# Performance work log

Measured on AMD Instinct MI355X. Metric: run time of the kernel, lower is better.

## Reference

```python
import jax, jax.numpy as jnp
import numpy as np

B, S, E, H = 4, 2048, 1024, 16
HD = E // H  # 64


def setup_inputs() -> dict:
    key = jax.random.key(0)
    k1, k2, k3, k4, k5 = jax.random.split(key, 5)
    scale = 0.02
    return {
        "hidden_states": jax.random.normal(k1, (B, S, E), dtype=jnp.float32),
        "c_attn_w": jax.random.normal(k2, (E, 3 * E), dtype=jnp.float32) * scale,
        "c_attn_b": jnp.zeros((3 * E,), dtype=jnp.float32),
        "c_proj_w": jax.random.normal(k3, (E, E), dtype=jnp.float32) * scale,
        "c_proj_b": jnp.zeros((E,), dtype=jnp.float32),
    }


def reference(hidden_states, c_attn_w, c_attn_b, c_proj_w, c_proj_b):
    b, s, e = hidden_states.shape
    h, hd = H, HD
    # Conv1D: x @ W + b
    qkv = hidden_states @ c_attn_w + c_attn_b                     # [B,S,3E]
    # Faithful to source: split heads BEFORE splitting q/k/v
    qkv = qkv.reshape(b, s, h, 3 * hd).transpose(0, 2, 1, 3)      # [B,H,S,3*hd]
    q, k, v = jnp.split(qkv, 3, axis=-1)                          # each [B,H,S,hd]
    scores = jnp.einsum("bhqd,bhkd->bhqk", q, k) / (hd ** 0.5)    # [B,H,S,S]
    causal = jnp.tril(jnp.ones((s, s), dtype=bool))
    masked_bias = jnp.asarray(-10000.0, dtype=scores.dtype)
    scores = jnp.where(causal, scores, masked_bias)
    attn_weights = jax.nn.softmax(scores, axis=-1)                # [B,H,S,S]
    attn_out = jnp.einsum("bhqk,bhkd->bhqd", attn_weights, v)     # [B,H,S,hd]
    attn_out = attn_out.transpose(0, 2, 1, 3).reshape(b, s, e)    # merge heads
    out = attn_out @ c_proj_w + c_proj_b                          # [B,S,E]
    return out
```

## Files before the change

kernel.cpp:

```cpp
#include <hip/hip_runtime.h>

typedef __attribute__((ext_vector_type(8))) __bf16 bf16x8;
typedef __attribute__((ext_vector_type(2))) __bf16 bf16x2;
typedef __attribute__((ext_vector_type(8))) unsigned short u16x8;
typedef __attribute__((ext_vector_type(4))) float f32x4;
typedef __attribute__((ext_vector_type(16))) float f32x16;
typedef __attribute__((ext_vector_type(4))) unsigned int u32x4;
typedef unsigned short u16;
typedef unsigned int u32;

constexpr int Bb = 4, Ss = 2048, Ee = 1024, Hh = 16, HDd = 64;
constexpr int Mm = Bb * Ss;
constexpr int N3 = 3 * Ee;
constexpr float QSC = 0.18033688011112042f;
constexpr int BHSTRIDE = Ss * HDd;
constexpr float M0 = 8.0f;

__device__ __forceinline__ u16 f2bf(float f) {
  u32 u = __builtin_bit_cast(u32, f);
  u = (u + 0x7FFFu + ((u >> 16) & 1u)) >> 16;
  return (u16)u;
}
__device__ __forceinline__ u32 pk2(float a, float b) {
  bf16x2 t;
  t[0] = (__bf16)a;
  t[1] = (__bf16)b;
  return __builtin_bit_cast(u32, t);
}
__device__ __forceinline__ float ex2(float x) { return __builtin_exp2f(x); }

__device__ __forceinline__ void gload_lds16(const void* g, void* l) {
  __builtin_amdgcn_global_load_lds(
      (__attribute__((address_space(1))) void*)g,
      (__attribute__((address_space(3))) void*)l, 16, 0, 0);
}

__device__ __forceinline__ f32x4 mfma16(bf16x8 a, bf16x8 b, f32x4 c) {
  return __builtin_amdgcn_mfma_f32_16x16x32_bf16(a, b, c, 0, 0, 0);
}
__device__ __forceinline__ f32x16 mfma32(bf16x8 a, bf16x8 b, f32x16 c) {
  return __builtin_amdgcn_mfma_f32_32x32x16_bf16(a, b, c, 0, 0, 0);
}

__global__ void cast_x_kernel(const float* __restrict__ x, u16* __restrict__ xb, int n4) {
  int i = blockIdx.x * blockDim.x + threadIdx.x;
  int stride = gridDim.x * blockDim.x;
  for (; i < n4; i += stride) {
    float4 v = reinterpret_cast<const float4*>(x)[i];
    ushort4 o;
    o.x = f2bf(v.x); o.y = f2bf(v.y); o.z = f2bf(v.z); o.w = f2bf(v.w);
    reinterpret_cast<ushort4*>(xb)[i] = o;
  }
}

__global__ void transpose_cast_kernel(const float* __restrict__ W, u16* __restrict__ Wt,
                                      int K, int N) {
  __shared__ float tile[32][33];
  int n0 = blockIdx.x * 32, k0 = blockIdx.y * 32;
  int tx = threadIdx.x & 31, ty = threadIdx.x >> 5;
#pragma unroll
  for (int i = 0; i < 4; ++i)
    tile[ty + i * 8][tx] = W[(size_t)(k0 + ty + i * 8) * N + n0 + tx];
  __syncthreads();
#pragma unroll
  for (int i = 0; i < 4; ++i)
    Wt[(size_t)(n0 + ty + i * 8) * K + k0 + tx] = f2bf(tile[tx][ty + i * 8]);
}

template <int MODE>
__global__ __launch_bounds__(512, 1) void gemm8_kernel(
    const u16* __restrict__ A, const u16* __restrict__ Bt,
    const float* __restrict__ bias, int xtiles, int cpx,
    float* __restrict__ Cout, u16* __restrict__ Qr,
    u16* __restrict__ Kp, u16* __restrict__ Vp) {
  extern __shared__ __attribute__((aligned(16))) u16 dyn[];
  constexpr int K = 1024, NT = 16;

  int f = blockIdx.x;
  int swz = (f & 7) * cpx + (f >> 3);
  int bx = swz % xtiles, by = swz / xtiles;
  int m0 = by * 128, n0 = bx * 256;

  int tid = threadIdx.x, lane = tid & 63, wid = tid >> 6;
  int wr = wid >> 2, wc = wid & 3;
  int l7 = lane & 7, l8 = lane >> 3;
  int swcol = (l7 ^ l8) * 8;

  const u16* Ab = A + (size_t)(m0 + l8) * K + swcol;
  const u16* Bb = Bt + (size_t)(n0 + l8) * K + swcol;

  f32x4 acc[4][4];
  const f32x4 fz = {0.f, 0.f, 0.f, 0.f};
#pragma unroll
  for (int mi = 0; mi < 4; ++mi)
#pragma unroll
    for (int nj = 0; nj < 4; ++nj) acc[mi][nj] = fz;

  auto stageA = [&](int tt, int c) {
    int ch = wid * 2 + c;
    gload_lds16(Ab + (size_t)(8 * ch) * K + tt * 64,
                dyn + (tt & 1) * 8192 + ch * 512);
  };
  auto stageB = [&](int tt, int c) {
    int ch = wid * 4 + c;
    gload_lds16(Bb + (size_t)(8 * ch) * K + tt * 64,
                dyn + 16384 + (tt & 1) * 16384 + ch * 512);
  };

  stageA(0, 0); stageA(0, 1);
  stageB(0, 0); stageB(0, 1); stageB(0, 2); stageB(0, 3);

  for (int t = 0; t < NT; ++t) {
    const u16* Ar = dyn + (t & 1) * 8192;
    const u16* Br = dyn + 16384 + (t & 1) * 16384;
    bool pre = (t + 1 < NT);
    if (pre) {
      stageA(t + 1, 0); stageA(t + 1, 1); stageB(t + 1, 0);
      asm volatile("s_waitcnt vmcnt(3)" ::: "memory");
    } else {
      asm volatile("s_waitcnt vmcnt(0)" ::: "memory");
    }
    __builtin_amdgcn_sched_barrier(0);
    __builtin_amdgcn_s_barrier();
    __builtin_amdgcn_sched_barrier(0);
#pragma unroll
    for (int kk = 0; kk < 2; ++kk) {
      if (kk == 1 && pre) { stageB(t + 1, 1); stageB(t + 1, 2); stageB(t + 1, 3); }
      bf16x8 af[4], bfr[4];
      int kc = kk * 4 + (lane >> 4);
      int jsw = (kc ^ l7) << 3;
#pragma unroll
      for (int i = 0; i < 4; ++i) {
        int rowA = wr * 64 + i * 16 + (lane & 15);
        af[i] = *(const bf16x8*)&Ar[rowA * 64 + jsw];
        int rowB = wc * 64 + i * 16 + (lane & 15);
        bfr[i] = *(const bf16x8*)&Br[rowB * 64 + jsw];
      }
      __builtin_amdgcn_s_setprio(1);
#pragma unroll
      for (int mi = 0; mi < 4; ++mi)
#pragma unroll
        for (int nj = 0; nj < 4; ++nj)
          acc[mi][nj] = mfma16(af[mi], bfr[nj], acc[mi][nj]);
      __builtin_amdgcn_s_setprio(0);
      asm volatile("" ::: "memory");
      __builtin_amdgcn_s_barrier();
      asm volatile("" ::: "memory");
    }
  }

  if (MODE == 0) {
    int Nn = xtiles * 256;
#pragma unroll
    for (int nj = 0; nj < 4; ++nj) {
      int n = n0 + wc * 64 + nj * 16 + (lane & 15);
      float bn = bias[n];
#pragma unroll
      for (int mi = 0; mi < 4; ++mi)
#pragma unroll
        for (int r = 0; r < 4; ++r) {
          int m = m0 + wr * 64 + mi * 16 + (lane >> 4) * 4 + r;
          Cout[(size_t)m * Nn + n] = acc[mi][nj][r] + bn;
        }
    }
  } else {
    int gidx = bx * 4 + wc;
    int typ = gidx % 3, h = gidx / 3;
    int bb = m0 >> 11;
    size_t basebh = (size_t)(bb * 16 + h) * BHSTRIDE;
    float cs = (typ == 0) ? QSC : 1.0f;
#pragma unroll
    for (int nj = 0; nj < 4; ++nj) {
      int dl = nj * 16 + (lane & 15);
      float bn = bias[gidx * 64 + dl];
#pragma unroll
      for (int mi = 0; mi < 4; ++mi)
#pragma unroll
        for (int r = 0; r < 4; ++r) {
          int m = m0 + wr * 64 + mi * 16 + (lane >> 4) * 4 + r;
          int srw = m & 2047;
          u16 v = f2bf((acc[mi][nj][r] + bn) * cs);
          if (typ == 0) {
            Qr[basebh + (size_t)srw * 64 + dl] = v;
          } else if (typ == 1) {
            int tile = srw >> 6, rl = srw & 63;
            Kp[basebh + tile * 4096 + (rl >> 5) * 2048 + (dl >> 4) * 512 +
               ((dl >> 3) & 1) * 256 + (rl & 31) * 8 + (dl & 7)] = v;
          } else {
            int tile = srw >> 6;
            Vp[basebh + tile * 4096 + (dl >> 5) * 2048 + ((srw >> 4) & 3) * 512 +
               ((srw >> 3) & 1) * 256 + (dl & 31) * 8 + (srw & 7)] = v;
          }
        }
    }
  }
}

__global__ __launch_bounds__(256) void attn_kernel(const u16* __restrict__ Qr,
                                                   const u16* __restrict__ Kp,
                                                   const u16* __restrict__ Vp,
                                                   u16* __restrict__ aout) {
  __shared__ float mbuf[2][64][33];

  int bh = blockIdx.x;
  int j = gridDim.y - 1 - blockIdx.y;
  int tid = threadIdx.x, w = tid >> 6, lane = tid & 63;
  int hi = lane >> 5, ln31 = lane & 31;
  int qrow = 32 * j + ln31;
  int nt = (j >> 1) + 1;
  int par = (j & 1) ? 32 : 0;

  size_t basebh = (size_t)bh * BHSTRIDE;
  const u16* kp = Kp + basebh + (size_t)w * 4096 + hi * 256 + ln31 * 8;
  const u16* vp = Vp + basebh + (size_t)w * 4096 + hi * 256 + ln31 * 8;

  bf16x8 qf[4];
#pragma unroll
  for (int kc = 0; kc < 4; ++kc)
    qf[kc] = *(const bf16x8*)(Qr + basebh + (size_t)qrow * 64 + kc * 16 + hi * 8);

  f32x16 o[2];
#pragma unroll
  for (int dm = 0; dm < 2; ++dm)
#pragma unroll
    for (int e = 0; e < 16; ++e) o[dm][e] = 0.f;
  float lrun = 0.f;

  for (int t = w; t < nt; t += 4, kp += 4 * 4096, vp += 4 * 4096) {
    bf16x8 kf[2][4], vf[2][4];
#pragma unroll
    for (int mt = 0; mt < 2; ++mt)
#pragma unroll
      for (int kc = 0; kc < 4; ++kc)
        kf[mt][kc] = *(const bf16x8*)(kp + mt * 2048 + kc * 512);
#pragma unroll
    for (int dm = 0; dm < 2; ++dm)
#pragma unroll
      for (int kw = 0; kw < 4; ++kw)
        vf[dm][kw] = *(const bf16x8*)(vp + dm * 2048 + kw * 512);

    f32x16 sc[2];
#pragma unroll
    for (int mt = 0; mt < 2; ++mt)
#pragma unroll
      for (int e = 0; e < 16; ++e) sc[mt][e] = 0.f;
    __builtin_amdgcn_s_setprio(1);
#pragma unroll
    for (int mt = 0; mt < 2; ++mt)
#pragma unroll
      for (int kc = 0; kc < 4; ++kc)
        sc[mt] = mfma32(kf[mt][kc], qf[kc], sc[mt]);
    __builtin_amdgcn_s_setprio(0);

    if (t == nt - 1) {
#pragma unroll
      for (int mt = 0; mt < 2; ++mt)
#pragma unroll
        for (int r = 0; r < 16; ++r) {
          bool msk = (32 * mt + (r & 3) + 8 * (r >> 2) + 4 * hi) > (ln31 + par);
          sc[mt][r] = msk ? -__builtin_inff() : sc[mt][r];
        }
    }
    float s0a = 0.f, s1a = 0.f, s2a = 0.f, s3a = 0.f;
#pragma unroll
    for (int mt = 0; mt < 2; ++mt)
#pragma unroll
      for (int r = 0; r < 16; ++r) {
        float e = ex2(sc[mt][r] - M0);
        sc[mt][r] = e;
        if ((r & 3) == 0) s0a += e;
        else if ((r & 3) == 1) s1a += e;
        else if ((r & 3) == 2) s2a += e;
        else s3a += e;
      }
    float sum = (s0a + s1a) + (s2a + s3a);
    sum += __shfl_xor(sum, 32);
    lrun += sum;

#pragma unroll
    for (int kw = 0; kw < 4; ++kw) {
      int mt = kw >> 1, k8 = (kw & 1) * 8;
      u32 a0 = pk2(sc[mt][k8 + 0], sc[mt][k8 + 1]);
      u32 a1 = pk2(sc[mt][k8 + 2], sc[mt][k8 + 3]);
      u32 b0 = pk2(sc[mt][k8 + 4], sc[mt][k8 + 5]);
      u32 b1 = pk2(sc[mt][k8 + 6], sc[mt][k8 + 7]);
      u32 s0 = hi ? a0 : b0;
      u32 s1 = hi ? a1 : b1;
      u32 r0 = (u32)__shfl_xor((int)s0, 32);
      u32 r1 = (u32)__shfl_xor((int)s1, 32);
      u32x4 fw;
      fw.x = hi ? r0 : a0;
      fw.y = hi ? r1 : a1;
      fw.z = hi ? b0 : r0;
      fw.w = hi ? b1 : r1;
      bf16x8 pf = __builtin_bit_cast(bf16x8, fw);
      __builtin_amdgcn_s_setprio(1);
#pragma unroll
      for (int dm = 0; dm < 2; ++dm)
        o[dm] = mfma32(vf[dm][kw], pf, o[dm]);
      __builtin_amdgcn_s_setprio(0);
    }
  }

  if (w >= 2) {
    mbuf[w - 2][lane][0] = lrun;
#pragma unroll
    for (int dm = 0; dm < 2; ++dm)
#pragma unroll
      for (int e = 0; e < 16; ++e) mbuf[w - 2][lane][1 + dm * 16 + e] = o[dm][e];
  }
  __syncthreads();
  if (w < 2) {
    lrun += mbuf[w][lane][0];
#pragma unroll
    for (int dm = 0; dm < 2; ++dm)
#pragma unroll
      for (int e = 0; e < 16; ++e) o[dm][e] += mbuf[w][lane][1 + dm * 16 + e];
  }
  __syncthreads();
  if (w == 1) {
    mbuf[0][lane][0] = lrun;
#pragma unroll
    for (int dm = 0; dm < 2; ++dm)
#pragma unroll
      for (int e = 0; e < 16; ++e) mbuf[0][lane][1 + dm * 16 + e] = o[dm][e];
  }
  __syncthreads();
  if (w == 0) {
    lrun += mbuf[0][lane][0];
#pragma unroll
    for (int dm = 0; dm < 2; ++dm)
#pragma unroll
      for (int e = 0; e < 16; ++e) o[dm][e] += mbuf[0][lane][1 + dm * 16 + e];
    int b = bh >> 4, h = bh & 15;
    float inv = 1.f / lrun;
    u16* orow = aout + (size_t)(b * Ss + qrow) * Ee + h * HDd;
#pragma unroll
    for (int dm = 0; dm < 2; ++dm)
#pragma unroll
      for (int g = 0; g < 4; ++g) {
        ushort4 st;
        st.x = f2bf(o[dm][4 * g + 0] * inv);
        st.y = f2bf(o[dm][4 * g + 1] * inv);
        st.z = f2bf(o[dm][4 * g + 2] * inv);
        st.w = f2bf(o[dm][4 * g + 3] * inv);
        *(ushort4*)(orow + 32 * dm + 8 * g + 4 * hi) = st;
      }
  }
}

extern "C" void kernel_launch(void* const* d_in, const int* in_sizes, int n_in,
                              void* d_out, int out_size, void* d_ws, size_t ws_size,
                              hipStream_t stream) {
  const float* hs        = (const float*)d_in[0];
  const float* c_attn_w  = (const float*)d_in[1];
  const float* c_attn_b  = (const float*)d_in[2];
  const float* c_proj_w  = (const float*)d_in[3];
  const float* c_proj_b  = (const float*)d_in[4];
  float* out = (float*)d_out;

  char* ws = (char*)d_ws;
  size_t off = 0;
  u16* xb     = (u16*)(ws + off); off += (size_t)Mm * Ee * 2;
  u16* wqkvt  = (u16*)(ws + off); off += (size_t)N3 * Ee * 2;
  u16* wprojt = (u16*)(ws + off); off += (size_t)Ee * Ee * 2;
  u16* Qr     = (u16*)(ws + off); off += (size_t)64 * BHSTRIDE * 2;
  u16* Kp     = (u16*)(ws + off); off += (size_t)64 * BHSTRIDE * 2;
  u16* Vp     = (u16*)(ws + off); off += (size_t)64 * BHSTRIDE * 2;
  u16* aoutb  = (u16*)(ws + off); off += (size_t)Mm * Ee * 2;
  if (ws_size < off) return;

  (void)hipFuncSetAttribute(reinterpret_cast<const void*>(gemm8_kernel<1>),
                            hipFuncAttributeMaxDynamicSharedMemorySize, 98304);
  (void)hipFuncSetAttribute(reinterpret_cast<const void*>(gemm8_kernel<0>),
                            hipFuncAttributeMaxDynamicSharedMemorySize, 98304);

  cast_x_kernel<<<2048, 256, 0, stream>>>(hs, xb, Mm * Ee / 4);
  transpose_cast_kernel<<<dim3(N3 / 32, Ee / 32), 256, 0, stream>>>(c_attn_w, wqkvt, Ee, N3);
  transpose_cast_kernel<<<dim3(Ee / 32, Ee / 32), 256, 0, stream>>>(c_proj_w, wprojt, Ee, Ee);
  gemm8_kernel<1><<<768, 512, 98304, stream>>>(
      xb, wqkvt, c_attn_b, 12, 96, nullptr, Qr, Kp, Vp);
  attn_kernel<<<dim3(Bb * Hh, 64), 256, 0, stream>>>(Qr, Kp, Vp, aoutb);
  gemm8_kernel<0><<<256, 512, 98304, stream>>>(
      aoutb, wprojt, c_proj_b, 4, 32, out, nullptr, nullptr, nullptr);
}
```

Before: 171.7 us.

## Triple-buffer GEMM LDS pipeline and stage QKV epilogue through LDS for vector stores

```diff
diff --git a/kernel.cpp b/kernel.cpp
--- a/kernel.cpp
+++ b/kernel.cpp
@@ -68,13 +68,14 @@
 }
 
 template <int MODE>
-__global__ __launch_bounds__(512, 1) void gemm8_kernel(
+__global__ __launch_bounds__(512, 1) void gemm_pipe(
     const u16* __restrict__ A, const u16* __restrict__ Bt,
     const float* __restrict__ bias, int xtiles, int cpx,
     float* __restrict__ Cout, u16* __restrict__ Qr,
     u16* __restrict__ Kp, u16* __restrict__ Vp) {
   extern __shared__ __attribute__((aligned(16))) u16 dyn[];
   constexpr int K = 1024, NT = 16;
+  constexpr int BUFSTRIDE = 24576;
 
   int f = blockIdx.x;
   int swz = (f & 7) * cpx + (f >> 3);
@@ -96,58 +97,68 @@
 #pragma unroll
     for (int nj = 0; nj < 4; ++nj) acc[mi][nj] = fz;
 
-  auto stageA = [&](int tt, int c) {
+  auto STA = [&](int tt, int c) {
     int ch = wid * 2 + c;
-    gload_lds16(Ab + (size_t)(8 * ch) * K + tt * 64,
-                dyn + (tt & 1) * 8192 + ch * 512);
+    gload_lds16(Ab + (size_t)(ch * 8) * K + tt * 64,
+                dyn + (tt % 3) * BUFSTRIDE + ch * 512);
   };
-  auto stageB = [&](int tt, int c) {
+  auto STB = [&](int tt, int c) {
     int ch = wid * 4 + c;
-    gload_lds16(Bb + (size_t)(8 * ch) * K + tt * 64,
-                dyn + 16384 + (tt & 1) * 16384 + ch * 512);
+    gload_lds16(Bb + (size_t)(ch * 8) * K + tt * 64,
+                dyn + (tt % 3) * BUFSTRIDE + 8192 + ch * 512);
   };
-
-  stageA(0, 0); stageA(0, 1);
-  stageB(0, 0); stageB(0, 1); stageB(0, 2); stageB(0, 3);
+  auto LDA = [&](const u16* buf, int mi, int ks) -> bf16x8 {
+    int row = wr * 64 + mi * 16 + (lane & 15);
+    int j = ((ks * 4 + (lane >> 4)) ^ l7) * 8;
+    return *(const bf16x8*)&buf[row * 64 + j];
+  };
+  auto LDB = [&](const u16* buf, int ni, int ks) -> bf16x8 {
+    int row = wc * 64 + ni * 16 + (lane & 15);
+    int j = ((ks * 4 + (lane >> 4)) ^ l7) * 8;
+    return *(const bf16x8*)&buf[row * 64 + j];
+  };
+
+#pragma unroll
+  for (int c = 0; c < 2; ++c) STA(0, c);
+#pragma unroll
+  for (int c = 0; c < 4; ++c) STB(0, c);
+#pragma unroll
+  for (int c = 0; c < 2; ++c) STA(1, c);
+#pragma unroll
+  for (int c = 0; c < 4; ++c) STB(1, c);
 
   for (int t = 0; t < NT; ++t) {
-    const u16* Ar = dyn + (t & 1) * 8192;
-    const u16* Br = dyn + 16384 + (t & 1) * 16384;
-    bool pre = (t + 1 < NT);
-    if (pre) {
-      stageA(t + 1, 0); stageA(t + 1, 1); stageB(t + 1, 0);
-      asm volatile("s_waitcnt vmcnt(3)" ::: "memory");
-    } else {
+    const u16* Ar = dyn + (t % 3) * BUFSTRIDE;
+    const u16* Br = Ar + 8192;
+    if (t + 1 < NT)
+      asm volatile("s_waitcnt vmcnt(6)" ::: "memory");
+    else
       asm volatile("s_waitcnt vmcnt(0)" ::: "memory");
-    }
     __builtin_amdgcn_sched_barrier(0);
     __builtin_amdgcn_s_barrier();
     __builtin_amdgcn_sched_barrier(0);
+
+    bool pre2 = (t + 2) < NT;
 #pragma unroll
     for (int kk = 0; kk < 2; ++kk) {
-      if (kk == 1 && pre) { stageB(t + 1, 1); stageB(t + 1, 2); stageB(t + 1, 3); }
       bf16x8 af[4], bfr[4];
-      int kc = kk * 4 + (lane >> 4);
-      int jsw = (kc ^ l7) << 3;
-#pragma unroll
-      for (int i = 0; i < 4; ++i) {
-        int rowA = wr * 64 + i * 16 + (lane & 15);
-        af[i] = *(const bf16x8*)&Ar[rowA * 64 + jsw];
-        int rowB = wc * 64 + i * 16 + (lane & 15);
-        bfr[i] = *(const bf16x8*)&Br[rowB * 64 + jsw];
-      }
+#pragma unroll
+      for (int mi = 0; mi < 4; ++mi) af[mi] = LDA(Ar, mi, kk);
+#pragma unroll
+      for (int ni = 0; ni < 4; ++ni) bfr[ni] = LDB(Br, ni, kk);
+      if (kk == 0 && pre2) { STA(t + 2, 0); STA(t + 2, 1); }
+      if (kk == 1 && pre2) { STB(t + 2, 0); STB(t + 2, 1); STB(t + 2, 2); STB(t + 2, 3); }
       __builtin_amdgcn_s_setprio(1);
 #pragma unroll
       for (int mi = 0; mi < 4; ++mi)
 #pragma unroll
-        for (int nj = 0; nj < 4; ++nj)
-          acc[mi][nj] = mfma16(af[mi], bfr[nj], acc[mi][nj]);
+        for (int ni = 0; ni < 4; ++ni)
+          acc[mi][ni] = mfma16(af[mi], bfr[ni], acc[mi][ni]);
       __builtin_amdgcn_s_setprio(0);
       asm volatile("" ::: "memory");
-      __builtin_amdgcn_s_barrier();
-      asm volatile("" ::: "memory");
     }
   }
+  __syncthreads();
 
   if (MODE == 0) {
     int Nn = xtiles * 256;
@@ -164,34 +175,68 @@
         }
     }
   } else {
-    int gidx = bx * 4 + wc;
-    int typ = gidx % 3, h = gidx / 3;
+    int gi0 = bx * 4;
     int bb = m0 >> 11;
-    size_t basebh = (size_t)(bb * 16 + h) * BHSTRIDE;
-    float cs = (typ == 0) ? QSC : 1.0f;
-#pragma unroll
-    for (int nj = 0; nj < 4; ++nj) {
-      int dl = nj * 16 + (lane & 15);
-      float bn = bias[gidx * 64 + dl];
-#pragma unroll
-      for (int mi = 0; mi < 4; ++mi)
-#pragma unroll
-        for (int r = 0; r < 4; ++r) {
-          int m = m0 + wr * 64 + mi * 16 + (lane >> 4) * 4 + r;
-          int srw = m & 2047;
-          u16 v = f2bf((acc[mi][nj][r] + bn) * cs);
-          if (typ == 0) {
-            Qr[basebh + (size_t)srw * 64 + dl] = v;
-          } else if (typ == 1) {
-            int tile = srw >> 6, rl = srw & 63;
-            Kp[basebh + tile * 4096 + (rl >> 5) * 2048 + (dl >> 4) * 512 +
-               ((dl >> 3) & 1) * 256 + (rl & 31) * 8 + (dl & 7)] = v;
-          } else {
-            int tile = srw >> 6;
-            Vp[basebh + tile * 4096 + (dl >> 5) * 2048 + ((srw >> 4) & 3) * 512 +
-               ((srw >> 3) & 1) * 256 + (dl & 31) * 8 + (srw & 7)] = v;
+    int mrow0 = m0 & 2047;
+#pragma unroll
+    for (int p = 0; p < 2; ++p) {
+      if ((wc >> 1) == p) {
+        int gg = wc & 1;
+        int gi = gi0 + p * 2 + gg;
+        int typ = gi % 3;
+        float cs = (typ == 0) ? QSC : 1.0f;
+#pragma unroll
+        for (int nj = 0; nj < 4; ++nj) {
+          int dl = nj * 16 + (lane & 15);
+          float bn = bias[gi * 64 + dl];
+#pragma unroll
+          for (int mi = 0; mi < 4; ++mi)
+#pragma unroll
+            for (int r = 0; r < 4; ++r) {
+              int row = wr * 64 + mi * 16 + (lane >> 4) * 4 + r;
+              dyn[(gg * 128 + row) * 72 + dl] = f2bf((acc[mi][nj][r] + bn) * cs);
+            }
+        }
+      }
+      __syncthreads();
+#pragma unroll
+      for (int gg = 0; gg < 2; ++gg) {
+        int gi = gi0 + p * 2 + gg;
+        int typ = gi % 3, h = gi / 3;
+        size_t basebh = (size_t)(bb * 16 + h) * BHSTRIDE;
+        if (typ == 2) {
+#pragma unroll
+          for (int i = 0; i < 2; ++i) {
+            int c = tid + 512 * i;
+            int dl = c & 63, s64 = (c >> 6) & 1, kv8 = c >> 7;
+            u16x8 val;
+            int lrow = gg * 128 + s64 * 64 + kv8 * 8;
+#pragma unroll
+            for (int e = 0; e < 8; ++e) val[e] = dyn[(lrow + e) * 72 + dl];
+            int tile = (mrow0 >> 6) + s64;
+            size_t o = basebh + (size_t)tile * 4096 + (dl >> 5) * 2048 +
+                       (kv8 >> 1) * 512 + (kv8 & 1) * 256 + (dl & 31) * 8;
+            *(u16x8*)(Vp + o) = val;
+          }
+        } else {
+#pragma unroll
+          for (int i = 0; i < 2; ++i) {
+            int c = tid + 512 * i;
+            int sl = c >> 3, dc = c & 7;
+            u16x8 val = *(const u16x8*)&dyn[(gg * 128 + sl) * 72 + dc * 8];
+            int srw = mrow0 + sl;
+            if (typ == 0) {
+              *(u16x8*)(Qr + basebh + (size_t)srw * 64 + dc * 8) = val;
+            } else {
+              int tile = srw >> 6, rl = srw & 63;
+              size_t o = basebh + (size_t)tile * 4096 + (rl >> 5) * 2048 +
+                         (dc >> 1) * 512 + (dc & 1) * 256 + (rl & 31) * 8;
+              *(u16x8*)(Kp + o) = val;
+            }
           }
         }
+      }
+      __syncthreads();
     }
   }
 }
@@ -370,17 +415,17 @@
   u16* aoutb  = (u16*)(ws + off); off += (size_t)Mm * Ee * 2;
   if (ws_size < off) return;
 
-  (void)hipFuncSetAttribute(reinterpret_cast<const void*>(gemm8_kernel<1>),
-                            hipFuncAttributeMaxDynamicSharedMemorySize, 98304);
-  (void)hipFuncSetAttribute(reinterpret_cast<const void*>(gemm8_kernel<0>),
-                            hipFuncAttributeMaxDynamicSharedMemorySize, 98304);
+  (void)hipFuncSetAttribute(reinterpret_cast<const void*>(gemm_pipe<1>),
+                            hipFuncAttributeMaxDynamicSharedMemorySize, 147456);
+  (void)hipFuncSetAttribute(reinterpret_cast<const void*>(gemm_pipe<0>),
+                            hipFuncAttributeMaxDynamicSharedMemorySize, 147456);
 
   cast_x_kernel<<<2048, 256, 0, stream>>>(hs, xb, Mm * Ee / 4);
   transpose_cast_kernel<<<dim3(N3 / 32, Ee / 32), 256, 0, stream>>>(c_attn_w, wqkvt, Ee, N3);
   transpose_cast_kernel<<<dim3(Ee / 32, Ee / 32), 256, 0, stream>>>(c_proj_w, wprojt, Ee, Ee);
-  gemm8_kernel<1><<<768, 512, 98304, stream>>>(
+  gemm_pipe<1><<<768, 512, 147456, stream>>>(
       xb, wqkvt, c_attn_b, 12, 96, nullptr, Qr, Kp, Vp);
   attn_kernel<<<dim3(Bb * Hh, 64), 256, 0, stream>>>(Qr, Kp, Vp, aoutb);
-  gemm8_kernel<0><<<256, 512, 98304, stream>>>(
+  gemm_pipe<0><<<256, 512, 147456, stream>>>(
       aoutb, wprojt, c_proj_b, 4, 32, out, nullptr, nullptr, nullptr);
 }
```

Result: faster. 162.2 us (-5.5%).
